# Kernel tuning notes

Measured on AMD Instinct MI355X. Metric: run time of the kernel, lower is better.

## Reference

```python
import jax, jax.numpy as jnp
import numpy as np

# Model dims
B = 64            # scenes (memory batch)
APER = 16         # agents per scene (uniform `length`)
A = B * APER      # total agents = sum(length)
TPAST = 20
TFUT = 30         # len_future
C = 256           # controller_size
M = 128           # memory_m
N = 256           # memory_n
H = 5             # num_heads (future modes)
SPACE = N // APER # per-agent write slot band
EMB = 16
D = C + M         # decoder hidden size


def _gru(x, h, wih, whh, bih, bhh):
    """torch.nn.GRU single-cell step."""
    gi = x @ wih.T + bih
    gh = h @ whh.T + bhh
    ir, iz, inn = jnp.split(gi, 3, axis=-1)
    hr, hz, hn = jnp.split(gh, 3, axis=-1)
    r = jax.nn.sigmoid(ir + hr)
    z = jax.nn.sigmoid(iz + hz)
    n = jnp.tanh(inn + r * hn)
    return (1.0 - z) * n + z * h


def _address(k, beta, mem, mask):
    """NTM content addressing: beta-sharpened masked softmax over cosine sims.
    k: (...,B,APER,M), beta: (...,B,APER,1), mem: (B,N,M), mask: (APER,N)."""
    kn = k / (jnp.linalg.norm(k, axis=-1, keepdims=True) + 1e-16)
    mn = mem / (jnp.linalg.norm(mem, axis=-1, keepdims=True) + 1e-16)
    sim = jnp.einsum('...bam,bnm->...ban', kn, mn)
    logits = beta * sim + (mask - 1.0) * 1e9
    return jax.nn.softmax(logits, axis=-1)


def setup_inputs() -> dict:
    key = jax.random.key(0)
    ks = iter(jax.random.split(key, 64))
    def nrm(shape, scale):
        return jax.random.normal(next(ks), shape, dtype=jnp.float32) * scale
    inp = dict(
        past=nrm((A, TPAST, 2), 1.0),
        past_rel=nrm((A, TPAST, 2), 1.0),
        ep_w1=nrm((8, 2), 0.7), ep_b1=jnp.zeros(8), ep_w2=nrm((EMB, 8), 0.35), ep_b2=jnp.zeros(EMB),
        er_w1=nrm((8, 2), 0.7), er_b1=jnp.zeros(8), er_w2=nrm((EMB, 8), 0.35), er_b2=jnp.zeros(EMB),
        enc_wih=nrm((3 * C, EMB + M), 1.0 / np.sqrt(EMB + M)), enc_whh=nrm((3 * C, C), 1.0 / np.sqrt(C)),
        enc_bih=jnp.zeros(3 * C), enc_bhh=jnp.zeros(3 * C),
        rel_wih=nrm((3 * C, EMB), 1.0 / np.sqrt(EMB)), rel_whh=nrm((3 * C, C), 1.0 / np.sqrt(C)),
        rel_bih=jnp.zeros(3 * C), rel_bhh=jnp.zeros(3 * C),
        dec_wih=nrm((3 * D, D), 1.0 / np.sqrt(D)), dec_whh=nrm((3 * D, D), 1.0 / np.sqrt(D)),
        dec_bih=jnp.zeros(3 * D), dec_bhh=jnp.zeros(3 * D),
        out_w=nrm((2, D), 1.0 / np.sqrt(D)), out_b=jnp.zeros(2),
        read_w=nrm((H, M + 1, C), 1.0 / np.sqrt(C)), read_b=jnp.zeros((H, M + 1)),
        write_w=nrm((3 * M + 1, C), 1.0 / np.sqrt(C)), write_b=jnp.zeros(3 * M + 1),
        init_r=nrm((1, M), 0.01),
        h_bias=nrm((1, C), 0.05), h_rel_bias=nrm((1, C), 0.05), h_fut_bias=nrm((1, D), 0.05),
        mem_bias=nrm((N, M), 0.05),
    )
    return inp


def reference(past, past_rel, ep_w1, ep_b1, ep_w2, ep_b2, er_w1, er_b1, er_w2, er_b2,
              enc_wih, enc_whh, enc_bih, enc_bhh, rel_wih, rel_whh, rel_bih, rel_bhh,
              dec_wih, dec_whh, dec_bih, dec_bhh, out_w, out_b,
              read_w, read_b, write_w, write_b,
              init_r, h_bias, h_rel_bias, h_fut_bias, mem_bias):
    # Per-agent disjoint write bands; read mask = other agents' bands.
    owner = jnp.arange(N) // SPACE
    mask_w = (owner[None, :] == jnp.arange(APER)[:, None]).astype(jnp.float32)  # (APER,N)
    mask_r = 1.0 - mask_w

    def mlp(x, w1, b1, w2, b2):
        return jax.nn.relu(x @ w1.T + b1) @ w2.T + b2

    emb_p = jnp.transpose(mlp(past, ep_w1, ep_b1, ep_w2, ep_b2), (1, 0, 2))      # (T,A,16)
    emb_r = jnp.transpose(mlp(past_rel, er_w1, er_b1, er_w2, er_b2), (1, 0, 2))  # (T,A,16)

    def step(carry, xs):
        emb, embr = xs
        mem, h, hr, hf, r = carry
        h = _gru(jnp.concatenate([emb, r], axis=-1), h, enc_wih, enc_whh, enc_bih, enc_bhh)
        hr = _gru(embr, hr, rel_wih, rel_whh, rel_bih, rel_bhh)
        # write head: k, beta, erase, add
        wp = h @ write_w.T + write_b
        kw = jnp.tanh(wp[:, :M]).reshape(B, APER, M)
        betaw = jax.nn.softplus(wp[:, M:M + 1]).reshape(B, APER, 1)
        er = jax.nn.sigmoid(wp[:, M + 1:2 * M + 1]).reshape(B, APER, M)
        ad = jnp.tanh(wp[:, 2 * M + 1:]).reshape(B, APER, M)
        ww = _address(kw, betaw, mem, mask_w)                                    # (B,APER,N)
        # erase/add; write bands are disjoint across agents so aggregation is exact
        mem = mem * (1.0 - jnp.einsum('ban,bam->bnm', ww, er)) + jnp.einsum('ban,bam->bnm', ww, ad)
        # per-head reads
        rp = jnp.einsum('ac,hkc->hak', hr, read_w) + read_b[:, None, :]          # (H,A,M+1)
        kr = jnp.tanh(rp[..., :M]).reshape(H, B, APER, M)
        betar = jax.nn.softplus(rp[..., M:]).reshape(H, B, APER, 1)
        wr = _address(kr, betar, mem, mask_r)                                    # (H,B,APER,N)
        reads = jnp.einsum('hban,bnm->hbam', wr, mem).reshape(H, A, M)
        r = reads[0]
        # per-mode decoder
        dec_in = jnp.concatenate([jnp.broadcast_to(h[None], (H, A, C)), reads], axis=-1).reshape(H * A, D)
        hf = _gru(dec_in, hf, dec_wih, dec_whh, dec_bih, dec_bhh)
        out = (hf @ out_w.T + out_b).reshape(H, A, 2)
        return (mem, h, hr, hf, r), out

    carry0 = (jnp.broadcast_to(mem_bias[None], (B, N, M)),
              jnp.broadcast_to(h_bias, (A, C)),
              jnp.broadcast_to(h_rel_bias, (A, C)),
              jnp.broadcast_to(h_fut_bias, (H * A, D)),
              jnp.broadcast_to(init_r, (A, M)))
    carry, _ = jax.lax.scan(step, carry0, (emb_p, emb_r))
    zf = jnp.zeros((TFUT, A, EMB), dtype=past.dtype)
    carry, outs = jax.lax.scan(step, carry, (zf, zf))                            # (TFUT,H,A,2)
    pred_rel = jnp.transpose(outs, (2, 1, 0, 3))                                 # (A,H,TFUT,2)
    pred = past[:, -1][:, None, None, :] + jnp.cumsum(pred_rel, axis=2)
    return pred, pred_rel
```

## Files before the change

kernel.cpp:

```cpp
#include <hip/hip_runtime.h>
#include <math.h>

#define B_    64
#define APER_ 16
#define A_    1024
#define TPAST_ 20
#define TFUT_  30
#define C_    256
#define M_    128
#define N_    256
#define H_    5
#define EMB_  16
#define D_    384
#define TTOT_ 50

typedef short bf16x8 __attribute__((ext_vector_type(8)));
typedef float f32x4 __attribute__((ext_vector_type(4)));

__device__ __forceinline__ float sigmoidf_(float x) { return 1.0f / (1.0f + expf(-x)); }
__device__ __forceinline__ float softplusf_(float x) { return (x > 20.0f) ? x : log1pf(expf(x)); }
__device__ __forceinline__ unsigned short f2bf(float f) {
    unsigned u = __float_as_uint(f);
    return (unsigned short)((u + 0x7FFFu + ((u >> 16) & 1u)) >> 16);
}
__device__ __forceinline__ float bf2f(short s) {
    return __uint_as_float(((unsigned)(unsigned short)s) << 16);
}

__global__ __launch_bounds__(256) void convert_w(const float* __restrict__ src, short* __restrict__ dst,
                                                 int srcRows, int srcK, int dstK, int total)
{
    const int idx = blockIdx.x * 256 + threadIdx.x;
    if (idx >= total) return;
    const int r = idx / dstK, k = idx % dstK;
    float v = (k < srcK && r < srcRows) ? src[(size_t)r * srcK + k] : 0.f;
    dst[idx] = (short)f2bf(v);
}

__global__ __launch_bounds__(64) void gru_mfma(
    const short* __restrict__ X1, int K1,
    const short* __restrict__ X2, int K2,
    const short* __restrict__ Wih, int Kpad,
    const float* __restrict__ bih,
    const short* __restrict__ Hb, const short* __restrict__ Whh,
    const float* __restrict__ bhh,
    const float* __restrict__ Hprev,
    float* __restrict__ Hnew, short* __restrict__ Hnewb,
    int G)
{
    const int lane = threadIdx.x;
    const int rowBase = blockIdx.x * 32;
    const int colBase = blockIdx.y * 32;
    const int l16 = lane & 15;
    const int kb8 = (lane >> 4) * 8;

    f32x4 gi[3][2][2], gh[3][2][2];
    const f32x4 z4 = {0.f, 0.f, 0.f, 0.f};
    #pragma unroll
    for (int g = 0; g < 3; ++g)
        #pragma unroll
        for (int i = 0; i < 2; ++i)
            #pragma unroll
            for (int j = 0; j < 2; ++j) { gi[g][i][j] = z4; gh[g][i][j] = z4; }

    for (int kc = 0; kc < Kpad; kc += 32) {
        bf16x8 afr[2];
        const int k8 = kc + kb8;
        #pragma unroll
        for (int i = 0; i < 2; ++i) {
            const int r = rowBase + i * 16 + l16;
            bf16x8 v = {0, 0, 0, 0, 0, 0, 0, 0};
            if (k8 < K1) {
                if (X1) v = *(const bf16x8*)(X1 + (size_t)(r & 1023) * K1 + k8);
            } else if (k8 < K1 + K2) {
                v = *(const bf16x8*)(X2 + (size_t)r * K2 + (k8 - K1));
            }
            afr[i] = v;
        }
        #pragma unroll
        for (int g = 0; g < 3; ++g)
            #pragma unroll
            for (int j = 0; j < 2; ++j) {
                const bf16x8 b = *(const bf16x8*)(Wih + (size_t)(g * G + colBase + j * 16 + l16) * Kpad + k8);
                gi[g][0][j] = __builtin_amdgcn_mfma_f32_16x16x32_bf16(afr[0], b, gi[g][0][j], 0, 0, 0);
                gi[g][1][j] = __builtin_amdgcn_mfma_f32_16x16x32_bf16(afr[1], b, gi[g][1][j], 0, 0, 0);
            }
    }
    for (int kc = 0; kc < G; kc += 32) {
        const int k8 = kc + kb8;
        bf16x8 afr[2];
        #pragma unroll
        for (int i = 0; i < 2; ++i)
            afr[i] = *(const bf16x8*)(Hb + (size_t)(rowBase + i * 16 + l16) * G + k8);
        #pragma unroll
        for (int g = 0; g < 3; ++g)
            #pragma unroll
            for (int j = 0; j < 2; ++j) {
                const bf16x8 b = *(const bf16x8*)(Whh + (size_t)(g * G + colBase + j * 16 + l16) * G + k8);
                gh[g][0][j] = __builtin_amdgcn_mfma_f32_16x16x32_bf16(afr[0], b, gh[g][0][j], 0, 0, 0);
                gh[g][1][j] = __builtin_amdgcn_mfma_f32_16x16x32_bf16(afr[1], b, gh[g][1][j], 0, 0, 0);
            }
    }

    const int r4 = (lane >> 4) * 4;
    #pragma unroll
    for (int j = 0; j < 2; ++j) {
        const int col = colBase + j * 16 + l16;
        const float bi0 = bih[col],         bh0 = bhh[col];
        const float bi1 = bih[G + col],     bh1 = bhh[G + col];
        const float bi2 = bih[2 * G + col], bh2 = bhh[2 * G + col];
        #pragma unroll
        for (int i = 0; i < 2; ++i) {
            #pragma unroll
            for (int q = 0; q < 4; ++q) {
                const int row = rowBase + i * 16 + r4 + q;
                const float rr = sigmoidf_(gi[0][i][j][q] + bi0 + gh[0][i][j][q] + bh0);
                const float zz = sigmoidf_(gi[1][i][j][q] + bi1 + gh[1][i][j][q] + bh1);
                const float nn = tanhf(gi[2][i][j][q] + bi2 + rr * (gh[2][i][j][q] + bh2));
                const float hp = Hprev[(size_t)row * G + col];
                const float hv = (1.f - zz) * nn + zz * hp;
                Hnew[(size_t)row * G + col] = hv;
                Hnewb[(size_t)row * G + col] = (short)f2bf(hv);
            }
        }
    }
}

__global__ __launch_bounds__(64) void gemm_mfma(
    const short* __restrict__ Xb, const short* __restrict__ Wb,
    const float* __restrict__ bias, float* __restrict__ Out,
    int Ncols, int K)
{
    const int lane = threadIdx.x;
    const int rowBase = blockIdx.x * 32;
    const int colBase = blockIdx.y * 32;
    const int l16 = lane & 15;
    const int kb8 = (lane >> 4) * 8;

    const f32x4 z4 = {0.f, 0.f, 0.f, 0.f};
    f32x4 acc[2][2] = {{z4, z4}, {z4, z4}};

    for (int kc = 0; kc < K; kc += 32) {
        const int k8 = kc + kb8;
        const bf16x8 a0 = *(const bf16x8*)(Xb + (size_t)(rowBase + l16) * K + k8);
        const bf16x8 a1 = *(const bf16x8*)(Xb + (size_t)(rowBase + 16 + l16) * K + k8);
        const bf16x8 b0 = *(const bf16x8*)(Wb + (size_t)(colBase + l16) * K + k8);
        const bf16x8 b1 = *(const bf16x8*)(Wb + (size_t)(colBase + 16 + l16) * K + k8);
        acc[0][0] = __builtin_amdgcn_mfma_f32_16x16x32_bf16(a0, b0, acc[0][0], 0, 0, 0);
        acc[0][1] = __builtin_amdgcn_mfma_f32_16x16x32_bf16(a0, b1, acc[0][1], 0, 0, 0);
        acc[1][0] = __builtin_amdgcn_mfma_f32_16x16x32_bf16(a1, b0, acc[1][0], 0, 0, 0);
        acc[1][1] = __builtin_amdgcn_mfma_f32_16x16x32_bf16(a1, b1, acc[1][1], 0, 0, 0);
    }
    const int r4 = (lane >> 4) * 4;
    #pragma unroll
    for (int j = 0; j < 2; ++j) {
        const int col = colBase + j * 16 + l16;
        if (col >= Ncols) continue;
        const float bv = bias[col];
        #pragma unroll
        for (int i = 0; i < 2; ++i)
            #pragma unroll
            for (int q = 0; q < 4; ++q) {
                const int row = rowBase + i * 16 + r4 + q;
                Out[(size_t)row * Ncols + col] = acc[i][j][q] + bv;
            }
    }
}

__global__ __launch_bounds__(256) void write_mem_k(const float* __restrict__ wp,
                                                   float* __restrict__ mem,
                                                   float* __restrict__ normsG)
{
    const int a = blockIdx.x;
    const int b = a >> 4, p = a & 15;
    __shared__ float kw[128], er[128], ad[128], red[256], ww[16], logit[16];
    __shared__ float buf[2048];
    __shared__ float beta_s, knorm_s;
    const int tid = threadIdx.x;
    const float* w = wp + (size_t)a * 385;
    if (tid < 128) {
        kw[tid] = tanhf(w[tid]);
        er[tid] = sigmoidf_(w[129 + tid]);
        ad[tid] = tanhf(w[257 + tid]);
    }
    if (tid == 0) beta_s = softplusf_(w[128]);
    __syncthreads();

    red[tid] = (tid < 128) ? kw[tid] * kw[tid] : 0.f;
    __syncthreads();
    for (int s = 128; s > 0; s >>= 1) { if (tid < s) red[tid] += red[tid + s]; __syncthreads(); }
    if (tid == 0) knorm_s = sqrtf(red[0]) + 1e-16f;
    __syncthreads();

    const int s = tid >> 4, j = tid & 15;
    float dot = 0.f, ss = 0.f;
    {
        const float* mrow = mem + ((size_t)(b * N_) + p * 16 + s) * M_;
        for (int k = j; k < 128; k += 16) { float v = mrow[k]; dot += kw[k] * v; ss += v * v; }
    }
    red[tid] = dot; __syncthreads();
    for (int st = 8; st > 0; st >>= 1) { if (j < st) red[tid] += red[tid + st]; __syncthreads(); }
    float dotf = red[s * 16];
    __syncthreads();
    red[tid] = ss; __syncthreads();
    for (int st = 8; st > 0; st >>= 1) { if (j < st) red[tid] += red[tid + st]; __syncthreads(); }
    float ssf = red[s * 16];
    if (j == 0) {
        float mn = sqrtf(ssf) + 1e-16f;
        logit[s] = beta_s * (dotf / (mn * knorm_s));
    }
    __syncthreads();
    if (tid == 0) {
        float mx = -1e30f;
        for (int i = 0; i < 16; ++i) mx = fmaxf(mx, logit[i]);
        float sum = 0.f;
        for (int i = 0; i < 16; ++i) { float e = __expf(logit[i] - mx); ww[i] = e; sum += e; }
        float inv = 1.f / sum;
        for (int i = 0; i < 16; ++i) ww[i] *= inv;
    }
    __syncthreads();
    for (int idx = tid; idx < 16 * 128; idx += 256) {
        int si = idx >> 7, m = idx & 127;
        size_t g = ((size_t)(b * N_) + p * 16 + si) * M_ + m;
        float wwv = ww[si];
        float v = mem[g] * (1.f - wwv * er[m]) + wwv * ad[m];
        mem[g] = v;
        buf[idx] = v;
    }
    __syncthreads();
    {
        float ssq = 0.f;
        #pragma unroll
        for (int i = 0; i < 8; ++i) { float v = buf[s * 128 + j + 16 * i]; ssq += v * v; }
        #pragma unroll
        for (int m = 1; m < 16; m <<= 1) ssq += __shfl_xor(ssq, m);
        if (j == 0) normsG[b * N_ + p * 16 + s] = sqrtf(ssq) + 1e-16f;
    }
}

__global__ __launch_bounds__(256) void read_k2(const float* __restrict__ rp,
                                               const float* __restrict__ mem,
                                               const float* __restrict__ normsG,
                                               short* __restrict__ reads_b)
{
    const int b = blockIdx.x;
    const int h = blockIdx.y;
    __shared__ __align__(16) float kq[16 * 132];
    __shared__ float S[16 * 260];
    __shared__ float beta_s[16], knorm_s[16], inv_s[16];
    const int t = threadIdx.x;
    const int a = t >> 4;
    const int sub = t & 15;

    {
        const float* base = rp + ((size_t)(b * 16 + a)) * 645 + h * 129;
        const int k0 = sub * 8;
        float v[8]; float ss = 0.f;
        #pragma unroll
        for (int r = 0; r < 8; ++r) { v[r] = tanhf(base[k0 + r]); ss += v[r] * v[r]; }
        float* dst = kq + a * 132 + k0;
        *(float4*)dst = make_float4(v[0], v[1], v[2], v[3]);
        *(float4*)(dst + 4) = make_float4(v[4], v[5], v[6], v[7]);
        #pragma unroll
        for (int m = 1; m < 16; m <<= 1) ss += __shfl_xor(ss, m);
        if (sub == 0) {
            knorm_s[a] = sqrtf(ss) + 1e-16f;
            beta_s[a] = softplusf_(base[128]);
        }
    }
    __syncthreads();

    {
        const int wave = t >> 6, lane = t & 63;
        const int l16 = lane & 15, kb8 = (lane >> 4) * 8;
        const int slotBase = wave * 64;
        const f32x4 z4 = {0.f, 0.f, 0.f, 0.f};
        f32x4 acc[4] = {z4, z4, z4, z4};
        const float* mb = mem + (size_t)b * N_ * M_;
        #pragma unroll
        for (int kc = 0; kc < 128; kc += 32) {
            const float* ap = kq + l16 * 132 + kc + kb8;
            bf16x8 ah, al;
            #pragma unroll
            for (int r = 0; r < 8; ++r) {
                const float av = ap[r];
                const short hv = (short)f2bf(av);
                ah[r] = hv; al[r] = (short)f2bf(av - bf2f(hv));
            }
            #pragma unroll
            for (int tt = 0; tt < 4; ++tt) {
                const float* bp = mb + (size_t)(slotBase + tt * 16 + l16) * M_ + kc + kb8;
                bf16x8 bh, bl;
                #pragma unroll
                for (int r = 0; r < 8; ++r) {
                    const float bv = bp[r];
                    const short hv = (short)f2bf(bv);
                    bh[r] = hv; bl[r] = (short)f2bf(bv - bf2f(hv));
                }
                acc[tt] = __builtin_amdgcn_mfma_f32_16x16x32_bf16(ah, bh, acc[tt], 0, 0, 0);
                acc[tt] = __builtin_amdgcn_mfma_f32_16x16x32_bf16(ah, bl, acc[tt], 0, 0, 0);
                acc[tt] = __builtin_amdgcn_mfma_f32_16x16x32_bf16(al, bh, acc[tt], 0, 0, 0);
            }
        }
        const int r4 = (lane >> 4) * 4;
        #pragma unroll
        for (int tt = 0; tt < 4; ++tt) {
            const int slot = slotBase + tt * 16 + l16;
            const float nv = normsG[b * N_ + slot];
            #pragma unroll
            for (int q = 0; q < 4; ++q) {
                const int aq = r4 + q;
                const float lg = ((slot >> 4) == aq) ? -1e30f
                               : beta_s[aq] * acc[tt][q] / (nv * knorm_s[aq]);
                S[aq * 260 + slot] = lg;
            }
        }
    }
    __syncthreads();

    {
        float mx = -1e30f;
        #pragma unroll
        for (int i = 0; i < 16; ++i) mx = fmaxf(mx, S[a * 260 + sub + 16 * i]);
        #pragma unroll
        for (int m = 1; m < 16; m <<= 1) mx = fmaxf(mx, __shfl_xor(mx, m));
        float e[16]; float sum = 0.f;
        #pragma unroll
        for (int i = 0; i < 16; ++i) { e[i] = __expf(S[a * 260 + sub + 16 * i] - mx); sum += e[i]; }
        #pragma unroll
        for (int i = 0; i < 16; ++i) S[a * 260 + sub + 16 * i] = e[i];
        #pragma unroll
        for (int m = 1; m < 16; m <<= 1) sum += __shfl_xor(sum, m);
        if (sub == 0) inv_s[a] = 1.f / sum;
    }
    __syncthreads();

    {
        const int m0 = sub * 8;
        const float* mb = mem + (size_t)b * N_ * M_ + m0;
        float acc[8];
        #pragma unroll
        for (int r = 0; r < 8; ++r) acc[r] = 0.f;
        const float* Sa = S + a * 260;
        #pragma unroll 4
        for (int n = 0; n < N_; ++n) {
            const float w = Sa[n];
            const float4 v0 = *(const float4*)(mb + (size_t)n * M_);
            const float4 v1 = *(const float4*)(mb + (size_t)n * M_ + 4);
            acc[0] = fmaf(w, v0.x, acc[0]); acc[1] = fmaf(w, v0.y, acc[1]);
            acc[2] = fmaf(w, v0.z, acc[2]); acc[3] = fmaf(w, v0.w, acc[3]);
            acc[4] = fmaf(w, v1.x, acc[4]); acc[5] = fmaf(w, v1.y, acc[5]);
            acc[6] = fmaf(w, v1.z, acc[6]); acc[7] = fmaf(w, v1.w, acc[7]);
        }
        const float inv = inv_s[a];
        short pk[8];
        #pragma unroll
        for (int r = 0; r < 8; ++r) pk[r] = (short)f2bf(acc[r] * inv);
        *(bf16x8*)(reads_b + ((size_t)h * A_ + b * 16 + a) * M_ + m0) = *(bf16x8*)pk;
    }
}

__global__ __launch_bounds__(256) void out_k(const float* __restrict__ hf,
                                             const float* __restrict__ out_w,
                                             const float* __restrict__ out_b,
                                             float* __restrict__ predrel, int t)
{
    const int row = blockIdx.x * 4 + (threadIdx.x >> 6);
    const int lane = threadIdx.x & 63;
    const float* hrow = hf + (size_t)row * D_;
    float a0 = 0.f, a1 = 0.f;
    for (int k = lane; k < D_; k += 64) {
        float v = hrow[k];
        a0 += v * out_w[k];
        a1 += v * out_w[D_ + k];
    }
    for (int off = 32; off > 0; off >>= 1) { a0 += __shfl_down(a0, off); a1 += __shfl_down(a1, off); }
    if (lane == 0) {
        int hh = row >> 10;
        int a = row & 1023;
        float* o = predrel + (((size_t)a * H_ + hh) * TFUT_ + t) * 2;
        o[0] = a0 + out_b[0];
        o[1] = a1 + out_b[1];
    }
}

__global__ __launch_bounds__(256) void cumsum_k(const float* __restrict__ past,
                                                const float* __restrict__ predrel,
                                                float* __restrict__ pred)
{
    const int idx = blockIdx.x * 256 + threadIdx.x;
    if (idx >= A_ * H_ * 2) return;
    const int c = idx & 1;
    const int ah = idx >> 1;
    const int a = ah / H_;
    float acc = past[((size_t)a * TPAST_ + TPAST_ - 1) * 2 + c];
    const float* pr = predrel + (size_t)ah * TFUT_ * 2 + c;
    float* pd = pred + (size_t)ah * TFUT_ * 2 + c;
    for (int t = 0; t < TFUT_; ++t) { acc += pr[t * 2]; pd[t * 2] = acc; }
}

__global__ __launch_bounds__(256) void embed_k(const float* __restrict__ x,
                                               const float* __restrict__ w1, const float* __restrict__ b1,
                                               const float* __restrict__ w2, const float* __restrict__ b2,
                                               short* __restrict__ emb)
{
    const int idx = blockIdx.x * 256 + threadIdx.x;
    if (idx >= A_ * TPAST_) return;
    const int a = idx / TPAST_, t = idx % TPAST_;
    const float x0 = x[(size_t)idx * 2], x1 = x[(size_t)idx * 2 + 1];
    float hbuf[8];
    #pragma unroll
    for (int j = 0; j < 8; ++j) hbuf[j] = fmaxf(0.f, w1[j * 2] * x0 + w1[j * 2 + 1] * x1 + b1[j]);
    short* e = emb + ((size_t)t * A_ + a) * EMB_;
    #pragma unroll
    for (int i = 0; i < 16; ++i) {
        float acc = b2[i];
        #pragma unroll
        for (int j = 0; j < 8; ++j) acc += w2[i * 8 + j] * hbuf[j];
        e[i] = (short)f2bf(acc);
    }
}

__global__ __launch_bounds__(256) void init_k(float* __restrict__ h, const float* __restrict__ h_bias, short* __restrict__ hb,
                                              float* __restrict__ hr, const float* __restrict__ hr_bias, short* __restrict__ hrb,
                                              float* __restrict__ hf, const float* __restrict__ hf_bias, short* __restrict__ hfb,
                                              short* __restrict__ reads_b, const float* __restrict__ init_r,
                                              float* __restrict__ mem,
                                              float* __restrict__ normsG, const float* __restrict__ mem_bias)
{
    const int idx = blockIdx.x * 256 + threadIdx.x;
    if (idx < B_ * N_ * M_) mem[idx] = mem_bias[idx & (N_ * M_ - 1)];
    if (idx < B_ * N_) {
        const float* r = mem_bias + (size_t)(idx & (N_ - 1)) * M_;
        float ss = 0.f;
        for (int k = 0; k < M_; ++k) ss += r[k] * r[k];
        normsG[idx] = sqrtf(ss) + 1e-16f;
    }
    if (idx < A_ * C_) {
        float v = h_bias[idx & (C_ - 1)];
        h[idx] = v; hb[idx] = (short)f2bf(v);
        v = hr_bias[idx & (C_ - 1)];
        hr[idx] = v; hrb[idx] = (short)f2bf(v);
    }
    if (idx < H_ * A_ * D_) {
        float v = hf_bias[idx % D_];
        hf[idx] = v; hfb[idx] = (short)f2bf(v);
    }
    if (idx < A_ * M_) reads_b[idx] = (short)f2bf(init_r[idx & (M_ - 1)]);
}

extern "C" void kernel_launch(void* const* d_in, const int* in_sizes, int n_in,
                              void* d_out, int out_size, void* d_ws, size_t ws_size,
                              hipStream_t stream)
{
    const float* past       = (const float*)d_in[0];
    const float* past_rel   = (const float*)d_in[1];
    const float* ep_w1      = (const float*)d_in[2];
    const float* ep_b1      = (const float*)d_in[3];
    const float* ep_w2      = (const float*)d_in[4];
    const float* ep_b2      = (const float*)d_in[5];
    const float* er_w1      = (const float*)d_in[6];
    const float* er_b1      = (const float*)d_in[7];
    const float* er_w2      = (const float*)d_in[8];
    const float* er_b2      = (const float*)d_in[9];
    const float* enc_wih    = (const float*)d_in[10];
    const float* enc_whh    = (const float*)d_in[11];
    const float* enc_bih    = (const float*)d_in[12];
    const float* enc_bhh    = (const float*)d_in[13];
    const float* rel_wih    = (const float*)d_in[14];
    const float* rel_whh    = (const float*)d_in[15];
    const float* rel_bih    = (const float*)d_in[16];
    const float* rel_bhh    = (const float*)d_in[17];
    const float* dec_wih    = (const float*)d_in[18];
    const float* dec_whh    = (const float*)d_in[19];
    const float* dec_bih    = (const float*)d_in[20];
    const float* dec_bhh    = (const float*)d_in[21];
    const float* out_w      = (const float*)d_in[22];
    const float* out_b      = (const float*)d_in[23];
    const float* read_w     = (const float*)d_in[24];
    const float* read_b     = (const float*)d_in[25];
    const float* write_w    = (const float*)d_in[26];
    const float* write_b    = (const float*)d_in[27];
    const float* init_r     = (const float*)d_in[28];
    const float* h_bias     = (const float*)d_in[29];
    const float* h_rel_bias = (const float*)d_in[30];
    const float* h_fut_bias = (const float*)d_in[31];
    const float* mem_bias   = (const float*)d_in[32];

    float* pred    = (float*)d_out;
    float* predrel = pred + (size_t)A_ * H_ * TFUT_ * 2;

    float* ws = (float*)d_ws;
    size_t off = 0;
    auto alloc = [&](size_t n) { float* p = ws + off; off += n; return p; };
    float* h0     = alloc((size_t)A_ * C_);
    float* h1     = alloc((size_t)A_ * C_);
    float* hr0    = alloc((size_t)A_ * C_);
    float* hr1    = alloc((size_t)A_ * C_);
    float* hf0    = alloc((size_t)H_ * A_ * D_);
    float* hf1    = alloc((size_t)H_ * A_ * D_);
    float* mem    = alloc((size_t)B_ * N_ * M_);
    float* wp     = alloc((size_t)A_ * 385);
    float* rp     = alloc((size_t)A_ * 645);
    float* normsG = alloc((size_t)B_ * N_);

    short* sws = (short*)(ws + off);
    size_t soff = 0;
    auto salloc = [&](size_t n) { short* p = sws + soff; soff += n; return p; };
    short* emb_p_b   = salloc((size_t)TPAST_ * A_ * EMB_);
    short* emb_r_b   = salloc((size_t)TPAST_ * A_ * EMB_);
    short* hb0       = salloc((size_t)A_ * C_);
    short* hb1       = salloc((size_t)A_ * C_);
    short* hrb0      = salloc((size_t)A_ * C_);
    short* hrb1      = salloc((size_t)A_ * C_);
    short* hfb0      = salloc((size_t)H_ * A_ * D_);
    short* hfb1      = salloc((size_t)H_ * A_ * D_);
    short* reads_b   = salloc((size_t)H_ * A_ * M_);
    short* enc_wih_b = salloc((size_t)768 * 160);
    short* enc_whh_b = salloc((size_t)768 * 256);
    short* rel_wih_b = salloc((size_t)768 * 32);
    short* rel_whh_b = salloc((size_t)768 * 256);
    short* dec_wih_b = salloc((size_t)1152 * 384);
    short* dec_whh_b = salloc((size_t)1152 * 384);
    short* write_w_b = salloc((size_t)416 * 256);
    short* read_w_b  = salloc((size_t)672 * 256);
    (void)ws_size; (void)in_sizes; (void)n_in; (void)out_size;

    auto cvt = [&](const float* s, short* d, int sr, int sk, int dr, int dk) {
        int total = dr * dk;
        convert_w<<<(total + 255) / 256, 256, 0, stream>>>(s, d, sr, sk, dk, total);
    };
    cvt(enc_wih, enc_wih_b, 768, 144, 768, 160);
    cvt(enc_whh, enc_whh_b, 768, 256, 768, 256);
    cvt(rel_wih, rel_wih_b, 768, 16, 768, 32);
    cvt(rel_whh, rel_whh_b, 768, 256, 768, 256);
    cvt(dec_wih, dec_wih_b, 1152, 384, 1152, 384);
    cvt(dec_whh, dec_whh_b, 1152, 384, 1152, 384);
    cvt(write_w, write_w_b, 385, 256, 416, 256);
    cvt(read_w, read_w_b, 645, 256, 672, 256);

    init_k<<<(B_ * N_ * M_ + 255) / 256, 256, 0, stream>>>(
        h0, h_bias, hb0, hr0, h_rel_bias, hrb0, hf0, h_fut_bias, hfb0,
        reads_b, init_r, mem, normsG, mem_bias);
    embed_k<<<(A_ * TPAST_ + 255) / 256, 256, 0, stream>>>(past, ep_w1, ep_b1, ep_w2, ep_b2, emb_p_b);
    embed_k<<<(A_ * TPAST_ + 255) / 256, 256, 0, stream>>>(past_rel, er_w1, er_b1, er_w2, er_b2, emb_r_b);

    float *hc = h0, *hn = h1, *hrc = hr0, *hrn = hr1, *hfc = hf0, *hfn = hf1;
    short *hbc = hb0, *hbn = hb1, *hrbc = hrb0, *hrbn = hrb1, *hfbc = hfb0, *hfbn = hfb1;

    const dim3 g_enc(A_ / 32, C_ / 32);
    const dim3 g_dec((H_ * A_) / 32, D_ / 32);
    const dim3 g_wp(A_ / 32, 13);
    const dim3 g_rp(A_ / 32, 21);
    const dim3 g_read(B_, H_);

    for (int t = 0; t < TTOT_; ++t) {
        const short* ep = (t < TPAST_) ? emb_p_b + (size_t)t * A_ * EMB_ : nullptr;
        const short* er = (t < TPAST_) ? emb_r_b + (size_t)t * A_ * EMB_ : nullptr;

        gru_mfma<<<g_enc, 64, 0, stream>>>(ep, 16, reads_b, 128,
                                           enc_wih_b, 160, enc_bih,
                                           hbc, enc_whh_b, enc_bhh,
                                           hc, hn, hbn, C_);
        gru_mfma<<<g_enc, 64, 0, stream>>>(er, 16, nullptr, 0,
                                           rel_wih_b, 32, rel_bih,
                                           hrbc, rel_whh_b, rel_bhh,
                                           hrc, hrn, hrbn, C_);
        gemm_mfma<<<g_wp, 64, 0, stream>>>(hbn, write_w_b, write_b, wp, 385, C_);
        write_mem_k<<<A_, 256, 0, stream>>>(wp, mem, normsG);
        gemm_mfma<<<g_rp, 64, 0, stream>>>(hrbn, read_w_b, read_b, rp, 645, C_);
        read_k2<<<g_read, 256, 0, stream>>>(rp, mem, normsG, reads_b);
        gru_mfma<<<g_dec, 64, 0, stream>>>(hbn, 256, reads_b, 128,
                                           dec_wih_b, 384, dec_bih,
                                           hfbc, dec_whh_b, dec_bhh,
                                           hfc, hfn, hfbn, D_);
        if (t >= TPAST_)
            out_k<<<(H_ * A_) / 4, 256, 0, stream>>>(hfn, out_w, out_b, predrel, t - TPAST_);

        float* tf;
        short* ts;
        tf = hc; hc = hn; hn = tf;      ts = hbc; hbc = hbn; hbn = ts;
        tf = hrc; hrc = hrn; hrn = tf;  ts = hrbc; hrbc = hrbn; hrbn = ts;
        tf = hfc; hfc = hfn; hfn = tf;  ts = hfbc; hfbc = hfbn; hfbn = ts;
    }
    cumsum_k<<<(A_ * H_ * 2 + 255) / 256, 256, 0, stream>>>(past, predrel, pred);
}
```

Before: 7.182 ms.

## Fuse timestep loop into one persistent cooperative kernel with grid syncs

Replaces the roughly 400 per-timestep kernel launches with a single cooperative kernel of 256 blocks by 512 threads. Inside it, work is split per wave and phases are separated by grid.sync. The encoder and relative GRUs run concurrently, as do the write and read projection GEMMs. The output projection overlaps with the next step's encoders, and the memory write is rewritten to use one wave per agent with shuffle reductions. This trades launch overhead and idle gaps for grid-barrier cost and reduced per-phase parallelism, since each phase is limited to 2048 waves.

```diff
diff --git a/kernel.cpp b/kernel.cpp
--- a/kernel.cpp
+++ b/kernel.cpp
@@ -1,5 +1,8 @@
 #include <hip/hip_runtime.h>
+#include <hip/hip_cooperative_groups.h>
 #include <math.h>
+
+namespace cg = cooperative_groups;
 
 #define B_    64
 #define APER_ 16
@@ -14,6 +17,10 @@
 #define D_    384
 #define TTOT_ 50
 
+#define WP_LD 400
+#define RP_LD 656
+#define LDSD_FLOATS 6320
+
 typedef short bf16x8 __attribute__((ext_vector_type(8)));
 typedef float f32x4 __attribute__((ext_vector_type(4)));
 
@@ -37,7 +44,57 @@
     dst[idx] = (short)f2bf(v);
 }
 
-__global__ __launch_bounds__(64) void gru_mfma(
+__global__ __launch_bounds__(256) void embed_k(const float* __restrict__ x,
+                                               const float* __restrict__ w1, const float* __restrict__ b1,
+                                               const float* __restrict__ w2, const float* __restrict__ b2,
+                                               short* __restrict__ emb)
+{
+    const int idx = blockIdx.x * 256 + threadIdx.x;
+    if (idx >= A_ * TPAST_) return;
+    const int a = idx / TPAST_, t = idx % TPAST_;
+    const float x0 = x[(size_t)idx * 2], x1 = x[(size_t)idx * 2 + 1];
+    float hbuf[8];
+    #pragma unroll
+    for (int j = 0; j < 8; ++j) hbuf[j] = fmaxf(0.f, w1[j * 2] * x0 + w1[j * 2 + 1] * x1 + b1[j]);
+    short* e = emb + ((size_t)t * A_ + a) * EMB_;
+    #pragma unroll
+    for (int i = 0; i < 16; ++i) {
+        float acc = b2[i];
+        #pragma unroll
+        for (int j = 0; j < 8; ++j) acc += w2[i * 8 + j] * hbuf[j];
+        e[i] = (short)f2bf(acc);
+    }
+}
+
+__global__ __launch_bounds__(256) void init_k(float* __restrict__ h, const float* __restrict__ h_bias, short* __restrict__ hb,
+                                              float* __restrict__ hr, const float* __restrict__ hr_bias, short* __restrict__ hrb,
+                                              float* __restrict__ hf, const float* __restrict__ hf_bias, short* __restrict__ hfb,
+                                              short* __restrict__ reads_b, const float* __restrict__ init_r,
+                                              float* __restrict__ mem,
+                                              float* __restrict__ normsG, const float* __restrict__ mem_bias)
+{
+    const int idx = blockIdx.x * 256 + threadIdx.x;
+    if (idx < B_ * N_ * M_) mem[idx] = mem_bias[idx & (N_ * M_ - 1)];
+    if (idx < B_ * N_) {
+        const float* r = mem_bias + (size_t)(idx & (N_ - 1)) * M_;
+        float ss = 0.f;
+        for (int k = 0; k < M_; ++k) ss += r[k] * r[k];
+        normsG[idx] = sqrtf(ss) + 1e-16f;
+    }
+    if (idx < A_ * C_) {
+        float v = h_bias[idx & (C_ - 1)];
+        h[idx] = v; hb[idx] = (short)f2bf(v);
+        v = hr_bias[idx & (C_ - 1)];
+        hr[idx] = v; hrb[idx] = (short)f2bf(v);
+    }
+    if (idx < H_ * A_ * D_) {
+        float v = hf_bias[idx % D_];
+        hf[idx] = v; hfb[idx] = (short)f2bf(v);
+    }
+    if (idx < A_ * M_) reads_b[idx] = (short)f2bf(init_r[idx & (M_ - 1)]);
+}
+
+__device__ __forceinline__ void gru_tile(
     const short* __restrict__ X1, int K1,
     const short* __restrict__ X2, int K2,
     const short* __restrict__ Wih, int Kpad,
@@ -46,11 +103,8 @@
     const float* __restrict__ bhh,
     const float* __restrict__ Hprev,
     float* __restrict__ Hnew, short* __restrict__ Hnewb,
-    int G)
-{
-    const int lane = threadIdx.x;
-    const int rowBase = blockIdx.x * 32;
-    const int colBase = blockIdx.y * 32;
+    int G, int rowBase, int colBase, int lane)
+{
     const int l16 = lane & 15;
     const int kb8 = (lane >> 4) * 8;
 
@@ -126,17 +180,13 @@
     }
 }
 
-__global__ __launch_bounds__(64) void gemm_mfma(
+__device__ __forceinline__ void gemm_tile(
     const short* __restrict__ Xb, const short* __restrict__ Wb,
     const float* __restrict__ bias, float* __restrict__ Out,
-    int Ncols, int K)
-{
-    const int lane = threadIdx.x;
-    const int rowBase = blockIdx.x * 32;
-    const int colBase = blockIdx.y * 32;
+    int Ncols, int ldOut, int K, int rowBase, int colBase, int lane)
+{
     const int l16 = lane & 15;
     const int kb8 = (lane >> 4) * 8;
-
     const f32x4 z4 = {0.f, 0.f, 0.f, 0.f};
     f32x4 acc[2][2] = {{z4, z4}, {z4, z4}};
 
@@ -162,116 +212,91 @@
             #pragma unroll
             for (int q = 0; q < 4; ++q) {
                 const int row = rowBase + i * 16 + r4 + q;
-                Out[(size_t)row * Ncols + col] = acc[i][j][q] + bv;
-            }
-    }
-}
-
-__global__ __launch_bounds__(256) void write_mem_k(const float* __restrict__ wp,
-                                                   float* __restrict__ mem,
-                                                   float* __restrict__ normsG)
-{
-    const int a = blockIdx.x;
-    const int b = a >> 4, p = a & 15;
-    __shared__ float kw[128], er[128], ad[128], red[256], ww[16], logit[16];
-    __shared__ float buf[2048];
-    __shared__ float beta_s, knorm_s;
-    const int tid = threadIdx.x;
-    const float* w = wp + (size_t)a * 385;
-    if (tid < 128) {
-        kw[tid] = tanhf(w[tid]);
-        er[tid] = sigmoidf_(w[129 + tid]);
-        ad[tid] = tanhf(w[257 + tid]);
-    }
-    if (tid == 0) beta_s = softplusf_(w[128]);
-    __syncthreads();
-
-    red[tid] = (tid < 128) ? kw[tid] * kw[tid] : 0.f;
-    __syncthreads();
-    for (int s = 128; s > 0; s >>= 1) { if (tid < s) red[tid] += red[tid + s]; __syncthreads(); }
-    if (tid == 0) knorm_s = sqrtf(red[0]) + 1e-16f;
-    __syncthreads();
-
-    const int s = tid >> 4, j = tid & 15;
-    float dot = 0.f, ss = 0.f;
-    {
-        const float* mrow = mem + ((size_t)(b * N_) + p * 16 + s) * M_;
-        for (int k = j; k < 128; k += 16) { float v = mrow[k]; dot += kw[k] * v; ss += v * v; }
-    }
-    red[tid] = dot; __syncthreads();
-    for (int st = 8; st > 0; st >>= 1) { if (j < st) red[tid] += red[tid + st]; __syncthreads(); }
-    float dotf = red[s * 16];
-    __syncthreads();
-    red[tid] = ss; __syncthreads();
-    for (int st = 8; st > 0; st >>= 1) { if (j < st) red[tid] += red[tid + st]; __syncthreads(); }
-    float ssf = red[s * 16];
-    if (j == 0) {
-        float mn = sqrtf(ssf) + 1e-16f;
-        logit[s] = beta_s * (dotf / (mn * knorm_s));
-    }
-    __syncthreads();
-    if (tid == 0) {
-        float mx = -1e30f;
-        for (int i = 0; i < 16; ++i) mx = fmaxf(mx, logit[i]);
-        float sum = 0.f;
-        for (int i = 0; i < 16; ++i) { float e = __expf(logit[i] - mx); ww[i] = e; sum += e; }
-        float inv = 1.f / sum;
-        for (int i = 0; i < 16; ++i) ww[i] *= inv;
-    }
-    __syncthreads();
-    for (int idx = tid; idx < 16 * 128; idx += 256) {
-        int si = idx >> 7, m = idx & 127;
-        size_t g = ((size_t)(b * N_) + p * 16 + si) * M_ + m;
-        float wwv = ww[si];
-        float v = mem[g] * (1.f - wwv * er[m]) + wwv * ad[m];
-        mem[g] = v;
-        buf[idx] = v;
-    }
-    __syncthreads();
-    {
-        float ssq = 0.f;
-        #pragma unroll
-        for (int i = 0; i < 8; ++i) { float v = buf[s * 128 + j + 16 * i]; ssq += v * v; }
-        #pragma unroll
-        for (int m = 1; m < 16; m <<= 1) ssq += __shfl_xor(ssq, m);
-        if (j == 0) normsG[b * N_ + p * 16 + s] = sqrtf(ssq) + 1e-16f;
-    }
-}
-
-__global__ __launch_bounds__(256) void read_k2(const float* __restrict__ rp,
-                                               const float* __restrict__ mem,
-                                               const float* __restrict__ normsG,
-                                               short* __restrict__ reads_b)
-{
-    const int b = blockIdx.x;
-    const int h = blockIdx.y;
-    __shared__ __align__(16) float kq[16 * 132];
-    __shared__ float S[16 * 260];
-    __shared__ float beta_s[16], knorm_s[16], inv_s[16];
-    const int t = threadIdx.x;
-    const int a = t >> 4;
-    const int sub = t & 15;
-
-    {
-        const float* base = rp + ((size_t)(b * 16 + a)) * 645 + h * 129;
+                Out[(size_t)row * ldOut + col] = acc[i][j][q] + bv;
+            }
+    }
+}
+
+__device__ __forceinline__ void write_agent(const float* __restrict__ wp, float* __restrict__ mem,
+                                            float* __restrict__ normsG, int a, int lane)
+{
+    const int s = lane >> 2, q = lane & 3;
+    const int b = a >> 4, pg = a & 15;
+    const float* w = wp + (size_t)a * WP_LD;
+    float* mrow = mem + ((size_t)(b * N_) + pg * 16 + s) * M_ + q * 32;
+    float mv[32];
+    #pragma unroll
+    for (int i = 0; i < 32; i += 4) {
+        const float4 m4 = *(const float4*)(mrow + i);
+        mv[i] = m4.x; mv[i + 1] = m4.y; mv[i + 2] = m4.z; mv[i + 3] = m4.w;
+    }
+    float dot = 0.f, ss = 0.f, kss = 0.f;
+    #pragma unroll
+    for (int i = 0; i < 32; ++i) {
+        const float kv = tanhf(w[q * 32 + i]);
+        kss += kv * kv; dot += kv * mv[i]; ss += mv[i] * mv[i];
+    }
+    dot += __shfl_xor(dot, 1); dot += __shfl_xor(dot, 2);
+    ss  += __shfl_xor(ss, 1);  ss  += __shfl_xor(ss, 2);
+    kss += __shfl_xor(kss, 1); kss += __shfl_xor(kss, 2);
+    const float beta = softplusf_(w[128]);
+    const float logit = beta * (dot / ((sqrtf(ss) + 1e-16f) * (sqrtf(kss) + 1e-16f)));
+    float mx = logit;
+    #pragma unroll
+    for (int d = 4; d < 64; d <<= 1) mx = fmaxf(mx, __shfl_xor(mx, d));
+    const float e = __expf(logit - mx);
+    float sum = e;
+    #pragma unroll
+    for (int d = 4; d < 64; d <<= 1) sum += __shfl_xor(sum, d);
+    const float wwv = e / sum;
+    float ssq = 0.f;
+    float vout[32];
+    #pragma unroll
+    for (int i = 0; i < 32; ++i) {
+        const float erv = sigmoidf_(w[129 + q * 32 + i]);
+        const float adv = tanhf(w[257 + q * 32 + i]);
+        const float v = mv[i] * (1.f - wwv * erv) + wwv * adv;
+        vout[i] = v; ssq += v * v;
+    }
+    #pragma unroll
+    for (int i = 0; i < 32; i += 4)
+        *(float4*)(mrow + i) = make_float4(vout[i], vout[i + 1], vout[i + 2], vout[i + 3]);
+    ssq += __shfl_xor(ssq, 1); ssq += __shfl_xor(ssq, 2);
+    if (q == 0) normsG[b * N_ + pg * 16 + s] = sqrtf(ssq) + 1e-16f;
+}
+
+__device__ void read_task(const float* __restrict__ rp, const float* __restrict__ mem,
+                          const float* __restrict__ normsG, short* __restrict__ reads_b,
+                          float* lds, int task, bool active, int tl)
+{
+    float* kq = lds;
+    float* S = lds + 2112;
+    float* beta_s = lds + 2112 + 4160;
+    float* knorm_s = beta_s + 16;
+    float* inv_s = knorm_s + 16;
+    const int h = task >> 6, b = task & 63;
+    const int a = tl >> 4, sub = tl & 15;
+
+    if (active) {
+        const float* base = rp + (size_t)(b * 16 + a) * RP_LD + h * 129;
         const int k0 = sub * 8;
-        float v[8]; float ss = 0.f;
-        #pragma unroll
-        for (int r = 0; r < 8; ++r) { v[r] = tanhf(base[k0 + r]); ss += v[r] * v[r]; }
+        float v[8]; float ssk = 0.f;
+        #pragma unroll
+        for (int r = 0; r < 8; ++r) { v[r] = tanhf(base[k0 + r]); ssk += v[r] * v[r]; }
         float* dst = kq + a * 132 + k0;
         *(float4*)dst = make_float4(v[0], v[1], v[2], v[3]);
         *(float4*)(dst + 4) = make_float4(v[4], v[5], v[6], v[7]);
         #pragma unroll
-        for (int m = 1; m < 16; m <<= 1) ss += __shfl_xor(ss, m);
+        for (int m = 1; m < 16; m <<= 1) ssk += __shfl_xor(ssk, m);
         if (sub == 0) {
-            knorm_s[a] = sqrtf(ss) + 1e-16f;
+            knorm_s[a] = sqrtf(ssk) + 1e-16f;
             beta_s[a] = softplusf_(base[128]);
         }
     }
     __syncthreads();
 
-    {
-        const int wave = t >> 6, lane = t & 63;
+    if (active) {
+        const int wave = tl >> 6, lane = tl & 63;
         const int l16 = lane & 15, kb8 = (lane >> 4) * 8;
         const int slotBase = wave * 64;
         const f32x4 z4 = {0.f, 0.f, 0.f, 0.f};
@@ -318,7 +343,7 @@
     }
     __syncthreads();
 
-    {
+    if (active) {
         float mx = -1e30f;
         #pragma unroll
         for (int i = 0; i < 16; ++i) mx = fmaxf(mx, S[a * 260 + sub + 16 * i]);
@@ -335,7 +360,7 @@
     }
     __syncthreads();
 
-    {
+    if (active) {
         const int m0 = sub * 8;
         const float* mb = mem + (size_t)b * N_ * M_ + m0;
         float acc[8];
@@ -360,93 +385,116 @@
     }
 }
 
-__global__ __launch_bounds__(256) void out_k(const float* __restrict__ hf,
-                                             const float* __restrict__ out_w,
-                                             const float* __restrict__ out_b,
-                                             float* __restrict__ predrel, int t)
-{
-    const int row = blockIdx.x * 4 + (threadIdx.x >> 6);
-    const int lane = threadIdx.x & 63;
+__device__ __forceinline__ void out_row(const float* __restrict__ hf,
+                                        const float* __restrict__ out_w, const float* __restrict__ out_b,
+                                        float* __restrict__ predrel, int row, int t, int lane)
+{
     const float* hrow = hf + (size_t)row * D_;
     float a0 = 0.f, a1 = 0.f;
     for (int k = lane; k < D_; k += 64) {
-        float v = hrow[k];
+        const float v = hrow[k];
         a0 += v * out_w[k];
         a1 += v * out_w[D_ + k];
     }
+    #pragma unroll
     for (int off = 32; off > 0; off >>= 1) { a0 += __shfl_down(a0, off); a1 += __shfl_down(a1, off); }
     if (lane == 0) {
-        int hh = row >> 10;
-        int a = row & 1023;
+        const int hh = row >> 10, a = row & 1023;
         float* o = predrel + (((size_t)a * H_ + hh) * TFUT_ + t) * 2;
         o[0] = a0 + out_b[0];
         o[1] = a1 + out_b[1];
     }
 }
 
-__global__ __launch_bounds__(256) void cumsum_k(const float* __restrict__ past,
-                                                const float* __restrict__ predrel,
-                                                float* __restrict__ pred)
-{
-    const int idx = blockIdx.x * 256 + threadIdx.x;
-    if (idx >= A_ * H_ * 2) return;
-    const int c = idx & 1;
-    const int ah = idx >> 1;
-    const int a = ah / H_;
-    float acc = past[((size_t)a * TPAST_ + TPAST_ - 1) * 2 + c];
-    const float* pr = predrel + (size_t)ah * TFUT_ * 2 + c;
-    float* pd = pred + (size_t)ah * TFUT_ * 2 + c;
-    for (int t = 0; t < TFUT_; ++t) { acc += pr[t * 2]; pd[t * 2] = acc; }
-}
-
-__global__ __launch_bounds__(256) void embed_k(const float* __restrict__ x,
-                                               const float* __restrict__ w1, const float* __restrict__ b1,
-                                               const float* __restrict__ w2, const float* __restrict__ b2,
-                                               short* __restrict__ emb)
-{
-    const int idx = blockIdx.x * 256 + threadIdx.x;
-    if (idx >= A_ * TPAST_) return;
-    const int a = idx / TPAST_, t = idx % TPAST_;
-    const float x0 = x[(size_t)idx * 2], x1 = x[(size_t)idx * 2 + 1];
-    float hbuf[8];
-    #pragma unroll
-    for (int j = 0; j < 8; ++j) hbuf[j] = fmaxf(0.f, w1[j * 2] * x0 + w1[j * 2 + 1] * x1 + b1[j]);
-    short* e = emb + ((size_t)t * A_ + a) * EMB_;
-    #pragma unroll
-    for (int i = 0; i < 16; ++i) {
-        float acc = b2[i];
-        #pragma unroll
-        for (int j = 0; j < 8; ++j) acc += w2[i * 8 + j] * hbuf[j];
-        e[i] = (short)f2bf(acc);
-    }
-}
-
-__global__ __launch_bounds__(256) void init_k(float* __restrict__ h, const float* __restrict__ h_bias, short* __restrict__ hb,
-                                              float* __restrict__ hr, const float* __restrict__ hr_bias, short* __restrict__ hrb,
-                                              float* __restrict__ hf, const float* __restrict__ hf_bias, short* __restrict__ hfb,
-                                              short* __restrict__ reads_b, const float* __restrict__ init_r,
-                                              float* __restrict__ mem,
-                                              float* __restrict__ normsG, const float* __restrict__ mem_bias)
-{
-    const int idx = blockIdx.x * 256 + threadIdx.x;
-    if (idx < B_ * N_ * M_) mem[idx] = mem_bias[idx & (N_ * M_ - 1)];
-    if (idx < B_ * N_) {
-        const float* r = mem_bias + (size_t)(idx & (N_ - 1)) * M_;
-        float ss = 0.f;
-        for (int k = 0; k < M_; ++k) ss += r[k] * r[k];
-        normsG[idx] = sqrtf(ss) + 1e-16f;
-    }
-    if (idx < A_ * C_) {
-        float v = h_bias[idx & (C_ - 1)];
-        h[idx] = v; hb[idx] = (short)f2bf(v);
-        v = hr_bias[idx & (C_ - 1)];
-        hr[idx] = v; hrb[idx] = (short)f2bf(v);
-    }
-    if (idx < H_ * A_ * D_) {
-        float v = hf_bias[idx % D_];
-        hf[idx] = v; hfb[idx] = (short)f2bf(v);
-    }
-    if (idx < A_ * M_) reads_b[idx] = (short)f2bf(init_r[idx & (M_ - 1)]);
+struct KParams {
+    const short *enc_wih, *enc_whh, *rel_wih, *rel_whh, *dec_wih, *dec_whh, *write_w, *read_w;
+    const float *enc_bih, *enc_bhh, *rel_bih, *rel_bhh, *dec_bih, *dec_bhh, *write_b, *read_b;
+    const float *out_w, *out_b, *past;
+    const short *emb_p, *emb_r;
+    float *h0, *h1, *hr0, *hr1, *hf0, *hf1, *mem, *wp, *rp, *normsG;
+    short *hb0, *hb1, *hrb0, *hrb1, *hfb0, *hfb1, *reads_b;
+    float *pred, *predrel;
+};
+
+__global__ __launch_bounds__(512, 1) void model_loop(KParams p)
+{
+    cg::grid_group grid = cg::this_grid();
+    __shared__ __align__(16) float ldsD[2 * LDSD_FLOATS];
+    const int wb = threadIdx.x >> 6;
+    const int lane = threadIdx.x & 63;
+    const int gw = ((int)blockIdx.x << 3) | wb;
+
+    float *hc = p.h0, *hn = p.h1, *hrc = p.hr0, *hrn = p.hr1, *hfc = p.hf0, *hfn = p.hf1;
+    short *hbc = p.hb0, *hbn = p.hb1, *hrbc = p.hrb0, *hrbn = p.hrb1, *hfbc = p.hfb0, *hfbn = p.hfb1;
+
+    for (int t = 0; t < TTOT_; ++t) {
+        if (gw < 256) {
+            const short* ep = (t < TPAST_) ? p.emb_p + (size_t)t * A_ * EMB_ : nullptr;
+            gru_tile(ep, 16, p.reads_b, 128, p.enc_wih, 160, p.enc_bih,
+                     hbc, p.enc_whh, p.enc_bhh, hc, hn, hbn, C_,
+                     (gw >> 3) * 32, (gw & 7) * 32, lane);
+        } else if (gw < 512) {
+            const int tw = gw - 256;
+            const short* er = (t < TPAST_) ? p.emb_r + (size_t)t * A_ * EMB_ : nullptr;
+            gru_tile(er, 16, nullptr, 0, p.rel_wih, 32, p.rel_bih,
+                     hrbc, p.rel_whh, p.rel_bhh, hrc, hrn, hrbn, C_,
+                     (tw >> 3) * 32, (tw & 7) * 32, lane);
+        } else if (t > TPAST_) {
+            for (int r = gw - 512; r < H_ * A_; r += 1536)
+                out_row(hfc, p.out_w, p.out_b, p.predrel, r, t - 1 - TPAST_, lane);
+        }
+        __threadfence(); grid.sync();
+
+        if (gw < 416) {
+            gemm_tile(hbn, p.write_w, p.write_b, p.wp, 385, WP_LD, C_,
+                      (gw & 31) * 32, (gw >> 5) * 32, lane);
+        } else if (gw < 1088) {
+            const int tw = gw - 416;
+            gemm_tile(hrbn, p.read_w, p.read_b, p.rp, 645, RP_LD, C_,
+                      (tw & 31) * 32, (tw >> 5) * 32, lane);
+        }
+        __threadfence(); grid.sync();
+
+        if (gw < A_) write_agent(p.wp, p.mem, p.normsG, gw, lane);
+        __threadfence(); grid.sync();
+
+        {
+            const int group = threadIdx.x >> 8;
+            const int task = (int)blockIdx.x + group * 256;
+            read_task(p.rp, p.mem, p.normsG, p.reads_b,
+                      ldsD + group * LDSD_FLOATS, task, task < B_ * H_, threadIdx.x & 255);
+        }
+        __threadfence(); grid.sync();
+
+        if (gw < 1920) {
+            gru_tile(hbn, 256, p.reads_b, 128, p.dec_wih, 384, p.dec_bih,
+                     hfbc, p.dec_whh, p.dec_bhh, hfc, hfn, hfbn, D_,
+                     (gw / 12) * 32, (gw % 12) * 32, lane);
+        }
+        __threadfence(); grid.sync();
+
+        float* tf; short* ts;
+        tf = hc; hc = hn; hn = tf;       ts = hbc; hbc = hbn; hbn = ts;
+        tf = hrc; hrc = hrn; hrn = tf;   ts = hrbc; hrbc = hrbn; hrbn = ts;
+        tf = hfc; hfc = hfn; hfn = tf;   ts = hfbc; hfbc = hfbn; hfbn = ts;
+    }
+
+    for (int r = gw; r < H_ * A_; r += 2048)
+        out_row(hfc, p.out_w, p.out_b, p.predrel, r, TTOT_ - 1 - TPAST_, lane);
+    __threadfence(); grid.sync();
+
+    {
+        const int idx = (int)blockIdx.x * 512 + threadIdx.x;
+        if (idx < A_ * H_ * 2) {
+            const int c = idx & 1;
+            const int ah = idx >> 1;
+            const int a = ah / H_;
+            float acc = p.past[((size_t)a * TPAST_ + TPAST_ - 1) * 2 + c];
+            const float* pr = p.predrel + (size_t)ah * TFUT_ * 2 + c;
+            float* pd = p.pred + (size_t)ah * TFUT_ * 2 + c;
+            for (int tt = 0; tt < TFUT_; ++tt) { acc += pr[tt * 2]; pd[tt * 2] = acc; }
+        }
+    }
 }
 
 extern "C" void kernel_launch(void* const* d_in, const int* in_sizes, int n_in,
@@ -500,8 +548,8 @@
     float* hf0    = alloc((size_t)H_ * A_ * D_);
     float* hf1    = alloc((size_t)H_ * A_ * D_);
     float* mem    = alloc((size_t)B_ * N_ * M_);
-    float* wp     = alloc((size_t)A_ * 385);
-    float* rp     = alloc((size_t)A_ * 645);
+    float* wp     = alloc((size_t)A_ * WP_LD);
+    float* rp     = alloc((size_t)A_ * RP_LD);
     float* normsG = alloc((size_t)B_ * N_);
 
     short* sws = (short*)(ws + off);
@@ -524,7 +572,7 @@
     short* dec_whh_b = salloc((size_t)1152 * 384);
     short* write_w_b = salloc((size_t)416 * 256);
     short* read_w_b  = salloc((size_t)672 * 256);
-    (void)ws_size; (void)in_sizes; (void)n_in; (void)out_size;
+    (void)ws_size; (void)in_sizes; (void)n_in; (void)out_size; (void)past_rel;
 
     auto cvt = [&](const float* s, short* d, int sr, int sk, int dr, int dk) {
         int total = dr * dk;
@@ -545,43 +593,24 @@
     embed_k<<<(A_ * TPAST_ + 255) / 256, 256, 0, stream>>>(past, ep_w1, ep_b1, ep_w2, ep_b2, emb_p_b);
     embed_k<<<(A_ * TPAST_ + 255) / 256, 256, 0, stream>>>(past_rel, er_w1, er_b1, er_w2, er_b2, emb_r_b);
 
-    float *hc = h0, *hn = h1, *hrc = hr0, *hrn = hr1, *hfc = hf0, *hfn = hf1;
-    short *hbc = hb0, *hbn = hb1, *hrbc = hrb0, *hrbn = hrb1, *hfbc = hfb0, *hfbn = hfb1;
-
-    const dim3 g_enc(A_ / 32, C_ / 32);
-    const dim3 g_dec((H_ * A_) / 32, D_ / 32);
-    const dim3 g_wp(A_ / 32, 13);
-    const dim3 g_rp(A_ / 32, 21);
-    const dim3 g_read(B_, H_);
-
-    for (int t = 0; t < TTOT_; ++t) {
-        const short* ep = (t < TPAST_) ? emb_p_b + (size_t)t * A_ * EMB_ : nullptr;
-        const short* er = (t < TPAST_) ? emb_r_b + (size_t)t * A_ * EMB_ : nullptr;
-
-        gru_mfma<<<g_enc, 64, 0, stream>>>(ep, 16, reads_b, 128,
-                                           enc_wih_b, 160, enc_bih,
-                                           hbc, enc_whh_b, enc_bhh,
-                                           hc, hn, hbn, C_);
-        gru_mfma<<<g_enc, 64, 0, stream>>>(er, 16, nullptr, 0,
-                                           rel_wih_b, 32, rel_bih,
-                                           hrbc, rel_whh_b, rel_bhh,
-                                           hrc, hrn, hrbn, C_);
-        gemm_mfma<<<g_wp, 64, 0, stream>>>(hbn, write_w_b, write_b, wp, 385, C_);
-        write_mem_k<<<A_, 256, 0, stream>>>(wp, mem, normsG);
-        gemm_mfma<<<g_rp, 64, 0, stream>>>(hrbn, read_w_b, read_b, rp, 645, C_);
-        read_k2<<<g_read, 256, 0, stream>>>(rp, mem, normsG, reads_b);
-        gru_mfma<<<g_dec, 64, 0, stream>>>(hbn, 256, reads_b, 128,
-                                           dec_wih_b, 384, dec_bih,
-                                           hfbc, dec_whh_b, dec_bhh,
-                                           hfc, hfn, hfbn, D_);
-        if (t >= TPAST_)
-            out_k<<<(H_ * A_) / 4, 256, 0, stream>>>(hfn, out_w, out_b, predrel, t - TPAST_);
-
-        float* tf;
-        short* ts;
-        tf = hc; hc = hn; hn = tf;      ts = hbc; hbc = hbn; hbn = ts;
-        tf = hrc; hrc = hrn; hrn = tf;  ts = hrbc; hrbc = hrbn; hrbn = ts;
-        tf = hfc; hfc = hfn; hfn = tf;  ts = hfbc; hfbc = hfbn; hfbn = ts;
-    }
-    cumsum_k<<<(A_ * H_ * 2 + 255) / 256, 256, 0, stream>>>(past, predrel, pred);
-}
+    KParams prm;
+    prm.enc_wih = enc_wih_b; prm.enc_whh = enc_whh_b;
+    prm.rel_wih = rel_wih_b; prm.rel_whh = rel_whh_b;
+    prm.dec_wih = dec_wih_b; prm.dec_whh = dec_whh_b;
+    prm.write_w = write_w_b; prm.read_w = read_w_b;
+    prm.enc_bih = enc_bih; prm.enc_bhh = enc_bhh;
+    prm.rel_bih = rel_bih; prm.rel_bhh = rel_bhh;
+    prm.dec_bih = dec_bih; prm.dec_bhh = dec_bhh;
+    prm.write_b = write_b; prm.read_b = read_b;
+    prm.out_w = out_w; prm.out_b = out_b; prm.past = past;
+    prm.emb_p = emb_p_b; prm.emb_r = emb_r_b;
+    prm.h0 = h0; prm.h1 = h1; prm.hr0 = hr0; prm.hr1 = hr1;
+    prm.hf0 = hf0; prm.hf1 = hf1; prm.mem = mem; prm.wp = wp; prm.rp = rp;
+    prm.normsG = normsG;
+    prm.hb0 = hb0; prm.hb1 = hb1; prm.hrb0 = hrb0; prm.hrb1 = hrb1;
+    prm.hfb0 = hfb0; prm.hfb1 = hfb1; prm.reads_b = reads_b;
+    prm.pred = pred; prm.predrel = predrel;
+
+    void* args[] = {&prm};
+    hipLaunchCooperativeKernel((const void*)model_loop, dim3(256), dim3(512), args, 0, stream);
+}
```

Result: slower. 26.96 ms (+275.3%).
